# Performance work log

Hardware: AMD Instinct MI355X
Metric: run time of the kernel (lower is better)

## Reference

```python
import jax, jax.numpy as jnp
import numpy as np

N = 262144  # total points
D = 256     # embedding dim
S = 8       # number of subbatches
L = 64      # instance labels per subbatch (label id range)
DELTA_V = 0.5
DELTA_D = 1.5


def setup_inputs() -> dict:
    key = jax.random.key(0)
    k1, k2, k3 = jax.random.split(key, 3)
    outputs = jax.random.normal(k1, (N, D), dtype=jnp.float32)
    labels = jax.random.randint(k2, (N,), 0, L, dtype=jnp.int32)
    subbatch_indices = jax.random.randint(k3, (N,), 0, S, dtype=jnp.int32)
    return {"outputs": outputs, "labels": labels, "subbatch_indices": subbatch_indices}


def reference(outputs, labels, subbatch_indices):
    n = outputs.shape[0]
    # normalize embeddings (L2 norm per point, matching torch.linalg.norm axis=1)
    x = outputs / (jnp.linalg.norm(outputs, axis=1) + 1e-8)[:, None]

    # combined segment id: (subbatch, label) -> subbatch*L + label
    seg = subbatch_indices * L + labels  # [N]
    num_seg = S * L

    ones = jnp.ones((n,), dtype=x.dtype)
    counts = jax.ops.segment_sum(ones, seg, num_segments=num_seg)        # [S*L] Nm per (sb,label)
    sums = jax.ops.segment_sum(x, seg, num_segments=num_seg)             # [S*L, D]
    mus = sums / jnp.maximum(counts, 1.0)[:, None]                        # centroids
    present = counts > 0                                                  # [S*L]
    M = jnp.sum(present.reshape(S, L).astype(x.dtype), axis=1)            # [S] unique labels per subbatch

    # ---- pull term: sum_m sum_{i in m} relu(||mu_m - x_i||_1 - dv)^2 / (M*Nm) ----
    mu_pt = mus[seg]                                                      # [N, D]
    d1 = jnp.sum(jnp.abs(mu_pt - x), axis=1)                              # [N] L1 dist to own centroid
    pull_pt = jax.nn.relu(d1 - DELTA_V) ** 2                              # weights are all 1.0
    denom = M[subbatch_indices] * counts[seg]                             # [N] M_sb * Nm
    L_pull = jax.ops.segment_sum(pull_pt / denom, subbatch_indices, num_segments=S)  # [S]

    # ---- push term: pairwise centroid L1 distances within each subbatch ----
    mus_s = mus.reshape(S, L, D)
    pres = present.reshape(S, L)
    dist = jnp.sum(jnp.abs(mus_s[:, :, None, :] - mus_s[:, None, :, :]), axis=-1)  # [S,L,L]
    pairmask = pres[:, :, None] & pres[:, None, :]
    pairmask = pairmask & (~jnp.eye(L, dtype=bool))[None]
    push = jnp.sum(jnp.where(pairmask, jax.nn.relu(2.0 * DELTA_D - dist) ** 2, 0.0), axis=(1, 2))
    L_push = push / jnp.maximum(M * (M - 1.0), 1.0)                        # [S]

    # only subbatches with M > 1 contribute; divide by B = total number of points
    valid = M > 1.0
    loss = jnp.sum(jnp.where(valid, L_pull + L_push, 0.0)) / n
    return loss
```

## Files before the change

### kernel.cpp

```cpp
#include <hip/hip_runtime.h>
#include <hip/hip_bf16.h>

#define DIM 256
#define NSB 8
#define NLBL 64
#define NSEG (NSB * NLBL)
#define BPS 4

__global__ void k_hist(const int* __restrict__ labels, const int* __restrict__ sbidx,
                       int* __restrict__ seg_out, int* __restrict__ counts, int n) {
    __shared__ int bins[NSEG];
    for (int i = threadIdx.x; i < NSEG; i += blockDim.x) bins[i] = 0;
    __syncthreads();
    int stride = gridDim.x * blockDim.x;
    for (int p = blockIdx.x * blockDim.x + threadIdx.x; p < n; p += stride) {
        int seg = sbidx[p] * NLBL + labels[p];
        seg_out[p] = seg;
        atomicAdd(&bins[seg], 1);
    }
    __syncthreads();
    for (int i = threadIdx.x; i < NSEG; i += blockDim.x)
        if (bins[i] > 0) atomicAdd(&counts[i], bins[i]);
}

__global__ void k_scan(const int* __restrict__ counts, int* __restrict__ offsets,
                       int* __restrict__ cursors, float* __restrict__ Mvals) {
    int lane = threadIdx.x;
    int carry = 0;
    for (int c = 0; c < NSB; c++) {
        int idx = c * 64 + lane;
        int v = counts[idx];
        int incl = v;
        #pragma unroll
        for (int m = 1; m < 64; m <<= 1) {
            int t = __shfl_up(incl, m, 64);
            if (lane >= m) incl += t;
        }
        int excl = carry + incl - v;
        offsets[idx] = excl;
        cursors[idx] = excl;
        carry += __shfl(incl, 63, 64);
        unsigned long long b = __ballot(v > 0);
        if (lane == 0) Mvals[c] = (float)__popcll(b);
    }
}

__global__ void k_scatter(const int* __restrict__ seg, int* __restrict__ cursors,
                          int* __restrict__ sorted, int n) {
    int stride = gridDim.x * blockDim.x;
    for (int p = blockIdx.x * blockDim.x + threadIdx.x; p < n; p += stride) {
        int pos = atomicAdd(&cursors[seg[p]], 1);
        sorted[pos] = p;
    }
}

__global__ void k_accum(const float* __restrict__ outp, const int* __restrict__ sorted,
                        const int* __restrict__ offsets, const int* __restrict__ counts,
                        float* __restrict__ partials) {
    int seg = blockIdx.x >> 2;
    int part = blockIdx.x & 3;
    int base = offsets[seg], cnt = counts[seg];
    int chunk = (cnt + BPS - 1) / BPS;
    int lo = base + part * chunk;
    int hi = min(base + cnt, lo + chunk);
    int wv = threadIdx.x >> 6, lane = threadIdx.x & 63;
    float4 acc = {0.f, 0.f, 0.f, 0.f};
    int i = lo + wv;
    int nextp = (i < hi) ? sorted[i] : 0;
    for (; i < hi; i += 4) {
        int p = nextp;
        int ni = i + 4;
        nextp = (ni < hi) ? sorted[ni] : 0;
        float4 v = *reinterpret_cast<const float4*>(outp + (size_t)p * DIM + lane * 4);
        float ss = v.x * v.x + v.y * v.y + v.z * v.z + v.w * v.w;
        #pragma unroll
        for (int m = 32; m >= 1; m >>= 1) ss += __shfl_xor(ss, m, 64);
        float rn = 1.0f / (sqrtf(ss) + 1e-8f);
        acc.x += v.x * rn; acc.y += v.y * rn; acc.z += v.z * rn; acc.w += v.w * rn;
    }
    __shared__ float pl[4][DIM];
    pl[wv][lane * 4 + 0] = acc.x;
    pl[wv][lane * 4 + 1] = acc.y;
    pl[wv][lane * 4 + 2] = acc.z;
    pl[wv][lane * 4 + 3] = acc.w;
    __syncthreads();
    int t = threadIdx.x;
    partials[(size_t)blockIdx.x * DIM + t] = pl[0][t] + pl[1][t] + pl[2][t] + pl[3][t];
}

__global__ void k_mu(const float* __restrict__ partials, const int* __restrict__ counts,
                     float* __restrict__ mus) {
    int seg = blockIdx.x, t = threadIdx.x;
    float s = 0.f;
    #pragma unroll
    for (int b = 0; b < BPS; b++) s += partials[((size_t)seg * BPS + b) * DIM + t];
    mus[(size_t)seg * DIM + t] = s / fmaxf((float)counts[seg], 1.0f);
}

__global__ void k_push(const float* __restrict__ mus, const int* __restrict__ counts,
                       float* __restrict__ pushv) {
    __shared__ float lds[NLBL][DIM + 1];
    int s = blockIdx.x >> 4;
    int chunk = blockIdx.x & 15;
    for (int i = threadIdx.x; i < NLBL * DIM; i += 256) {
        int r = i >> 8, d = i & 255;
        lds[r][d] = mus[((size_t)s * NLBL + r) * DIM + d];
    }
    __syncthreads();
    int pair = chunk * 256 + threadIdx.x;
    int l1 = pair >> 6, l2 = pair & 63;
    float dist = 0.0f;
    #pragma unroll 8
    for (int d = 0; d < DIM; d++) dist += fabsf(lds[l1][d] - lds[l2][d]);
    float v = fmaxf(3.0f - dist, 0.0f);
    v = v * v;
    bool ok = (l1 != l2) && (counts[s * NLBL + l1] > 0) && (counts[s * NLBL + l2] > 0);
    v = ok ? v : 0.0f;
    #pragma unroll
    for (int m = 32; m >= 1; m >>= 1) v += __shfl_xor(v, m, 64);
    __shared__ float wsum[4];
    if ((threadIdx.x & 63) == 0) wsum[threadIdx.x >> 6] = v;
    __syncthreads();
    if (threadIdx.x == 0) atomicAdd(&pushv[s], wsum[0] + wsum[1] + wsum[2] + wsum[3]);
}

__global__ void k_pull(const float* __restrict__ outp, const int* __restrict__ sorted,
                       const int* __restrict__ offsets, const int* __restrict__ counts,
                       const float* __restrict__ mus, const float* __restrict__ Mvals,
                       float* __restrict__ Lpull) {
    int seg = blockIdx.x >> 2;
    int part = blockIdx.x & 3;
    int sb = seg >> 6;
    int base = offsets[seg], cnt = counts[seg];
    if (cnt == 0) return;
    int chunk = (cnt + BPS - 1) / BPS;
    int lo = base + part * chunk;
    int hi = min(base + cnt, lo + chunk);
    int wv = threadIdx.x >> 6, lane = threadIdx.x & 63;
    float4 mu = *reinterpret_cast<const float4*>(mus + (size_t)seg * DIM + lane * 4);
    float psum = 0.f;
    int i = lo + wv;
    int nextp = (i < hi) ? sorted[i] : 0;
    for (; i < hi; i += 4) {
        int p = nextp;
        int ni = i + 4;
        nextp = (ni < hi) ? sorted[ni] : 0;
        float4 v = *reinterpret_cast<const float4*>(outp + (size_t)p * DIM + lane * 4);
        float ss = v.x * v.x + v.y * v.y + v.z * v.z + v.w * v.w;
        #pragma unroll
        for (int m = 32; m >= 1; m >>= 1) ss += __shfl_xor(ss, m, 64);
        float rn = 1.0f / (sqrtf(ss) + 1e-8f);
        float d1 = fabsf(mu.x - v.x * rn) + fabsf(mu.y - v.y * rn) +
                   fabsf(mu.z - v.z * rn) + fabsf(mu.w - v.w * rn);
        #pragma unroll
        for (int m = 32; m >= 1; m >>= 1) d1 += __shfl_xor(d1, m, 64);
        float t = fmaxf(d1 - 0.5f, 0.0f);
        psum += t * t;
    }
    __shared__ float wsum[4];
    if (lane == 0) wsum[wv] = psum;
    __syncthreads();
    if (threadIdx.x == 0) {
        float tot = wsum[0] + wsum[1] + wsum[2] + wsum[3];
        atomicAdd(&Lpull[sb], tot / (Mvals[sb] * (float)cnt));
    }
}

__global__ void k_final(const float* __restrict__ Lpull, const float* __restrict__ pushv,
                        const float* __restrict__ Mvals, float* __restrict__ outv, int n) {
    if (threadIdx.x == 0 && blockIdx.x == 0) {
        float loss = 0.0f;
        for (int s = 0; s < NSB; s++) {
            float M = Mvals[s];
            if (M > 1.0f)
                loss += Lpull[s] + pushv[s] / fmaxf(M * (M - 1.0f), 1.0f);
        }
        outv[0] = loss / (float)n;
    }
}

extern "C" void kernel_launch(void* const* d_in, const int* in_sizes, int n_in,
                              void* d_out, int out_size, void* d_ws, size_t ws_size,
                              hipStream_t stream) {
    const float* outp = (const float*)d_in[0];
    const int* labels = (const int*)d_in[1];
    const int* sbidx = (const int*)d_in[2];
    float* out = (float*)d_out;
    int n = in_sizes[1];

    float* mus = (float*)d_ws;
    float* partials = mus + (size_t)NSEG * DIM;
    int* seg = (int*)(partials + (size_t)NSEG * BPS * DIM);
    int* sorted = seg + n;
    int* counts = sorted + n;
    float* Lpull = (float*)(counts + NSEG);
    float* pushv = Lpull + NSB;
    int* offsets = (int*)(pushv + NSB);
    int* cursors = offsets + NSEG;
    float* Mvals = (float*)(cursors + NSEG);

    hipMemsetAsync(counts, 0, (NSEG + 2 * NSB) * 4, stream);

    k_hist<<<256, 256, 0, stream>>>(labels, sbidx, seg, counts, n);
    k_scan<<<1, 64, 0, stream>>>(counts, offsets, cursors, Mvals);
    k_scatter<<<512, 256, 0, stream>>>(seg, cursors, sorted, n);
    k_accum<<<NSEG * BPS, 256, 0, stream>>>(outp, sorted, offsets, counts, partials);
    k_mu<<<NSEG, DIM, 0, stream>>>(partials, counts, mus);
    k_push<<<NSB * 16, 256, 0, stream>>>(mus, counts, pushv);
    k_pull<<<NSEG * BPS, 256, 0, stream>>>(outp, sorted, offsets, counts, mus, Mvals, Lpull);
    k_final<<<1, 64, 0, stream>>>(Lpull, pushv, Mvals, out, n);
}
```

Baseline: 226.1 us.

## Fuse scan into histogram, merge mu into push, stream pull over points linearly

The prefix scan moves into the histogram kernel using a last-block-done counter, which removes one launch and the seg array write. The histogram and scatter now read labels and subbatch indices directly with int4 vector loads. Centroid finalisation is folded into the push kernel. The pull kernel now reads the embedding matrix sequentially instead of gathering through the sorted index, and normalises per point with precomputed inverse counts. Accum and pull each process two points per wave iteration for more memory-level parallelism. The costs are extra work in the push blocks and LDS atomics in pull.

```diff
diff --git a/kernel.cpp b/kernel.cpp
--- a/kernel.cpp
+++ b/kernel.cpp
@@ -8,49 +8,69 @@
 #define BPS 4
 
 __global__ void k_hist(const int* __restrict__ labels, const int* __restrict__ sbidx,
-                       int* __restrict__ seg_out, int* __restrict__ counts, int n) {
+                       int* __restrict__ counts, int* __restrict__ done,
+                       int* __restrict__ offsets, int* __restrict__ cursors,
+                       float* __restrict__ Mvals, float* __restrict__ invcnt, int n) {
     __shared__ int bins[NSEG];
+    __shared__ int lastFlag;
     for (int i = threadIdx.x; i < NSEG; i += blockDim.x) bins[i] = 0;
     __syncthreads();
-    int stride = gridDim.x * blockDim.x;
-    for (int p = blockIdx.x * blockDim.x + threadIdx.x; p < n; p += stride) {
-        int seg = sbidx[p] * NLBL + labels[p];
-        seg_out[p] = seg;
-        atomicAdd(&bins[seg], 1);
+    int t4 = blockIdx.x * blockDim.x + threadIdx.x;
+    int stride4 = gridDim.x * blockDim.x;
+    for (int q = t4; q * 4 < n; q += stride4) {
+        int4 lb = reinterpret_cast<const int4*>(labels)[q];
+        int4 sb = reinterpret_cast<const int4*>(sbidx)[q];
+        atomicAdd(&bins[sb.x * NLBL + lb.x], 1);
+        atomicAdd(&bins[sb.y * NLBL + lb.y], 1);
+        atomicAdd(&bins[sb.z * NLBL + lb.z], 1);
+        atomicAdd(&bins[sb.w * NLBL + lb.w], 1);
     }
     __syncthreads();
     for (int i = threadIdx.x; i < NSEG; i += blockDim.x)
         if (bins[i] > 0) atomicAdd(&counts[i], bins[i]);
-}
-
-__global__ void k_scan(const int* __restrict__ counts, int* __restrict__ offsets,
-                       int* __restrict__ cursors, float* __restrict__ Mvals) {
-    int lane = threadIdx.x;
-    int carry = 0;
-    for (int c = 0; c < NSB; c++) {
-        int idx = c * 64 + lane;
-        int v = counts[idx];
-        int incl = v;
-        #pragma unroll
-        for (int m = 1; m < 64; m <<= 1) {
-            int t = __shfl_up(incl, m, 64);
-            if (lane >= m) incl += t;
-        }
-        int excl = carry + incl - v;
-        offsets[idx] = excl;
-        cursors[idx] = excl;
-        carry += __shfl(incl, 63, 64);
-        unsigned long long b = __ballot(v > 0);
-        if (lane == 0) Mvals[c] = (float)__popcll(b);
-    }
-}
-
-__global__ void k_scatter(const int* __restrict__ seg, int* __restrict__ cursors,
-                          int* __restrict__ sorted, int n) {
+    __syncthreads();
+    if (threadIdx.x == 0) {
+        __threadfence();
+        int t = atomicAdd(done, 1);
+        lastFlag = (t == (int)gridDim.x - 1) ? 1 : 0;
+    }
+    __syncthreads();
+    if (!lastFlag) return;
+    if (threadIdx.x < 64) {
+        int lane = threadIdx.x;
+        int carry = 0;
+        for (int c = 0; c < NSB; c++) {
+            int idx = c * 64 + lane;
+            int v = atomicAdd(&counts[idx], 0);
+            int incl = v;
+            #pragma unroll
+            for (int m = 1; m < 64; m <<= 1) {
+                int t2 = __shfl_up(incl, m, 64);
+                if (lane >= m) incl += t2;
+            }
+            int excl = carry + incl - v;
+            offsets[idx] = excl;
+            cursors[idx] = excl;
+            invcnt[idx] = 1.0f / fmaxf((float)v, 1.0f);
+            carry += __shfl(incl, 63, 64);
+            unsigned long long b = __ballot(v > 0);
+            if (lane == 0) Mvals[c] = (float)__popcll(b);
+        }
+    }
+}
+
+__global__ void k_scatter(const int* __restrict__ labels, const int* __restrict__ sbidx,
+                          int* __restrict__ cursors, int* __restrict__ sorted, int n) {
+    int t = blockIdx.x * blockDim.x + threadIdx.x;
     int stride = gridDim.x * blockDim.x;
-    for (int p = blockIdx.x * blockDim.x + threadIdx.x; p < n; p += stride) {
-        int pos = atomicAdd(&cursors[seg[p]], 1);
-        sorted[pos] = p;
+    for (int q = t; q * 4 < n; q += stride) {
+        int4 lb = reinterpret_cast<const int4*>(labels)[q];
+        int4 sb = reinterpret_cast<const int4*>(sbidx)[q];
+        int p = q * 4;
+        sorted[atomicAdd(&cursors[sb.x * NLBL + lb.x], 1)] = p;
+        sorted[atomicAdd(&cursors[sb.y * NLBL + lb.y], 1)] = p + 1;
+        sorted[atomicAdd(&cursors[sb.z * NLBL + lb.z], 1)] = p + 2;
+        sorted[atomicAdd(&cursors[sb.w * NLBL + lb.w], 1)] = p + 3;
     }
 }
 
@@ -65,18 +85,31 @@
     int hi = min(base + cnt, lo + chunk);
     int wv = threadIdx.x >> 6, lane = threadIdx.x & 63;
     float4 acc = {0.f, 0.f, 0.f, 0.f};
-    int i = lo + wv;
-    int nextp = (i < hi) ? sorted[i] : 0;
-    for (; i < hi; i += 4) {
-        int p = nextp;
-        int ni = i + 4;
-        nextp = (ni < hi) ? sorted[ni] : 0;
-        float4 v = *reinterpret_cast<const float4*>(outp + (size_t)p * DIM + lane * 4);
-        float ss = v.x * v.x + v.y * v.y + v.z * v.z + v.w * v.w;
+    int i = lo + wv * 2;
+    int p0 = (i < hi) ? sorted[i] : -1;
+    int p1 = (i + 1 < hi) ? sorted[i + 1] : -1;
+    for (; i < hi; i += 8) {
+        int ni = i + 8;
+        int np0 = (ni < hi) ? sorted[ni] : -1;
+        int np1 = (ni + 1 < hi) ? sorted[ni + 1] : -1;
+        float4 v0 = {0.f, 0.f, 0.f, 0.f}, v1 = {0.f, 0.f, 0.f, 0.f};
+        v0 = *reinterpret_cast<const float4*>(outp + (size_t)p0 * DIM + lane * 4);
+        if (p1 >= 0)
+            v1 = *reinterpret_cast<const float4*>(outp + (size_t)p1 * DIM + lane * 4);
+        float ss0 = v0.x * v0.x + v0.y * v0.y + v0.z * v0.z + v0.w * v0.w;
+        float ss1 = v1.x * v1.x + v1.y * v1.y + v1.z * v1.z + v1.w * v1.w;
         #pragma unroll
-        for (int m = 32; m >= 1; m >>= 1) ss += __shfl_xor(ss, m, 64);
-        float rn = 1.0f / (sqrtf(ss) + 1e-8f);
-        acc.x += v.x * rn; acc.y += v.y * rn; acc.z += v.z * rn; acc.w += v.w * rn;
+        for (int m = 32; m >= 1; m >>= 1) {
+            ss0 += __shfl_xor(ss0, m, 64);
+            ss1 += __shfl_xor(ss1, m, 64);
+        }
+        float rn0 = 1.0f / (sqrtf(ss0) + 1e-8f);
+        float rn1 = 1.0f / (sqrtf(ss1) + 1e-8f);
+        acc.x += v0.x * rn0 + v1.x * rn1;
+        acc.y += v0.y * rn0 + v1.y * rn1;
+        acc.z += v0.z * rn0 + v1.z * rn1;
+        acc.w += v0.w * rn0 + v1.w * rn1;
+        p0 = np0; p1 = np1;
     }
     __shared__ float pl[4][DIM];
     pl[wv][lane * 4 + 0] = acc.x;
@@ -88,23 +121,19 @@
     partials[(size_t)blockIdx.x * DIM + t] = pl[0][t] + pl[1][t] + pl[2][t] + pl[3][t];
 }
 
-__global__ void k_mu(const float* __restrict__ partials, const int* __restrict__ counts,
-                     float* __restrict__ mus) {
-    int seg = blockIdx.x, t = threadIdx.x;
-    float s = 0.f;
-    #pragma unroll
-    for (int b = 0; b < BPS; b++) s += partials[((size_t)seg * BPS + b) * DIM + t];
-    mus[(size_t)seg * DIM + t] = s / fmaxf((float)counts[seg], 1.0f);
-}
-
-__global__ void k_push(const float* __restrict__ mus, const int* __restrict__ counts,
-                       float* __restrict__ pushv) {
+__global__ void k_push(const float* __restrict__ partials, const int* __restrict__ counts,
+                       float* __restrict__ mus, float* __restrict__ pushv) {
     __shared__ float lds[NLBL][DIM + 1];
     int s = blockIdx.x >> 4;
     int chunk = blockIdx.x & 15;
     for (int i = threadIdx.x; i < NLBL * DIM; i += 256) {
         int r = i >> 8, d = i & 255;
-        lds[r][d] = mus[((size_t)s * NLBL + r) * DIM + d];
+        int segid = s * NLBL + r;
+        const float* pp = partials + (size_t)segid * BPS * DIM + d;
+        float sum = pp[0] + pp[DIM] + pp[2 * DIM] + pp[3 * DIM];
+        float mu = sum / fmaxf((float)counts[segid], 1.0f);
+        lds[r][d] = mu;
+        if (chunk == 0) mus[(size_t)segid * DIM + d] = mu;
     }
     __syncthreads();
     int pair = chunk * 256 + threadIdx.x;
@@ -124,46 +153,55 @@
     if (threadIdx.x == 0) atomicAdd(&pushv[s], wsum[0] + wsum[1] + wsum[2] + wsum[3]);
 }
 
-__global__ void k_pull(const float* __restrict__ outp, const int* __restrict__ sorted,
-                       const int* __restrict__ offsets, const int* __restrict__ counts,
-                       const float* __restrict__ mus, const float* __restrict__ Mvals,
-                       float* __restrict__ Lpull) {
-    int seg = blockIdx.x >> 2;
-    int part = blockIdx.x & 3;
-    int sb = seg >> 6;
-    int base = offsets[seg], cnt = counts[seg];
-    if (cnt == 0) return;
-    int chunk = (cnt + BPS - 1) / BPS;
-    int lo = base + part * chunk;
-    int hi = min(base + cnt, lo + chunk);
-    int wv = threadIdx.x >> 6, lane = threadIdx.x & 63;
-    float4 mu = *reinterpret_cast<const float4*>(mus + (size_t)seg * DIM + lane * 4);
-    float psum = 0.f;
-    int i = lo + wv;
-    int nextp = (i < hi) ? sorted[i] : 0;
-    for (; i < hi; i += 4) {
-        int p = nextp;
-        int ni = i + 4;
-        nextp = (ni < hi) ? sorted[ni] : 0;
-        float4 v = *reinterpret_cast<const float4*>(outp + (size_t)p * DIM + lane * 4);
-        float ss = v.x * v.x + v.y * v.y + v.z * v.z + v.w * v.w;
+__global__ void k_pull(const float* __restrict__ outp, const int* __restrict__ labels,
+                       const int* __restrict__ sbidx, const float* __restrict__ mus,
+                       const float* __restrict__ invcnt, float* __restrict__ Lpull, int n) {
+    __shared__ float lp[NSB];
+    if (threadIdx.x < NSB) lp[threadIdx.x] = 0.f;
+    __syncthreads();
+    int gtid = blockIdx.x * blockDim.x + threadIdx.x;
+    int w = gtid >> 6;
+    int lane = threadIdx.x & 63;
+    int nw = (gridDim.x * blockDim.x) >> 6;
+    for (int p0 = w * 2; p0 < n; p0 += nw * 2) {
+        int p1 = p0 + 1;
+        bool has1 = p1 < n;
+        float4 x0 = *reinterpret_cast<const float4*>(outp + (size_t)p0 * DIM + lane * 4);
+        float4 x1 = {0.f, 0.f, 0.f, 0.f};
+        if (has1) x1 = *reinterpret_cast<const float4*>(outp + (size_t)p1 * DIM + lane * 4);
+        int seg0 = sbidx[p0] * NLBL + labels[p0];
+        int seg1 = has1 ? (sbidx[p1] * NLBL + labels[p1]) : 0;
+        float4 mu0 = *reinterpret_cast<const float4*>(mus + (size_t)seg0 * DIM + lane * 4);
+        float4 mu1 = *reinterpret_cast<const float4*>(mus + (size_t)seg1 * DIM + lane * 4);
+        float ss0 = x0.x * x0.x + x0.y * x0.y + x0.z * x0.z + x0.w * x0.w;
+        float ss1 = x1.x * x1.x + x1.y * x1.y + x1.z * x1.z + x1.w * x1.w;
         #pragma unroll
-        for (int m = 32; m >= 1; m >>= 1) ss += __shfl_xor(ss, m, 64);
-        float rn = 1.0f / (sqrtf(ss) + 1e-8f);
-        float d1 = fabsf(mu.x - v.x * rn) + fabsf(mu.y - v.y * rn) +
-                   fabsf(mu.z - v.z * rn) + fabsf(mu.w - v.w * rn);
+        for (int m = 32; m >= 1; m >>= 1) {
+            ss0 += __shfl_xor(ss0, m, 64);
+            ss1 += __shfl_xor(ss1, m, 64);
+        }
+        float rn0 = 1.0f / (sqrtf(ss0) + 1e-8f);
+        float rn1 = 1.0f / (sqrtf(ss1) + 1e-8f);
+        float d10 = fabsf(mu0.x - x0.x * rn0) + fabsf(mu0.y - x0.y * rn0) +
+                    fabsf(mu0.z - x0.z * rn0) + fabsf(mu0.w - x0.w * rn0);
+        float d11 = fabsf(mu1.x - x1.x * rn1) + fabsf(mu1.y - x1.y * rn1) +
+                    fabsf(mu1.z - x1.z * rn1) + fabsf(mu1.w - x1.w * rn1);
         #pragma unroll
-        for (int m = 32; m >= 1; m >>= 1) d1 += __shfl_xor(d1, m, 64);
-        float t = fmaxf(d1 - 0.5f, 0.0f);
-        psum += t * t;
-    }
-    __shared__ float wsum[4];
-    if (lane == 0) wsum[wv] = psum;
-    __syncthreads();
-    if (threadIdx.x == 0) {
-        float tot = wsum[0] + wsum[1] + wsum[2] + wsum[3];
-        atomicAdd(&Lpull[sb], tot / (Mvals[sb] * (float)cnt));
-    }
+        for (int m = 32; m >= 1; m >>= 1) {
+            d10 += __shfl_xor(d10, m, 64);
+            d11 += __shfl_xor(d11, m, 64);
+        }
+        if (lane == 0) {
+            float t0 = fmaxf(d10 - 0.5f, 0.f);
+            atomicAdd(&lp[seg0 >> 6], t0 * t0 * invcnt[seg0]);
+            if (has1) {
+                float t1 = fmaxf(d11 - 0.5f, 0.f);
+                atomicAdd(&lp[seg1 >> 6], t1 * t1 * invcnt[seg1]);
+            }
+        }
+    }
+    __syncthreads();
+    if (threadIdx.x < NSB) atomicAdd(&Lpull[threadIdx.x], lp[threadIdx.x]);
 }
 
 __global__ void k_final(const float* __restrict__ Lpull, const float* __restrict__ pushv,
@@ -173,7 +211,7 @@
         for (int s = 0; s < NSB; s++) {
             float M = Mvals[s];
             if (M > 1.0f)
-                loss += Lpull[s] + pushv[s] / fmaxf(M * (M - 1.0f), 1.0f);
+                loss += Lpull[s] / M + pushv[s] / fmaxf(M * (M - 1.0f), 1.0f);
         }
         outv[0] = loss / (float)n;
     }
@@ -188,25 +226,24 @@
     float* out = (float*)d_out;
     int n = in_sizes[1];
 
-    float* mus = (float*)d_ws;
-    float* partials = mus + (size_t)NSEG * DIM;
-    int* seg = (int*)(partials + (size_t)NSEG * BPS * DIM);
-    int* sorted = seg + n;
+    float* partials = (float*)d_ws;
+    float* mus = partials + (size_t)NSEG * BPS * DIM;
+    int* sorted = (int*)(mus + (size_t)NSEG * DIM);
     int* counts = sorted + n;
-    float* Lpull = (float*)(counts + NSEG);
+    int* done = counts + NSEG;
+    float* Lpull = (float*)(done + 1);
     float* pushv = Lpull + NSB;
     int* offsets = (int*)(pushv + NSB);
     int* cursors = offsets + NSEG;
     float* Mvals = (float*)(cursors + NSEG);
-
-    hipMemsetAsync(counts, 0, (NSEG + 2 * NSB) * 4, stream);
-
-    k_hist<<<256, 256, 0, stream>>>(labels, sbidx, seg, counts, n);
-    k_scan<<<1, 64, 0, stream>>>(counts, offsets, cursors, Mvals);
-    k_scatter<<<512, 256, 0, stream>>>(seg, cursors, sorted, n);
+    float* invcnt = Mvals + NSB;
+
+    hipMemsetAsync(counts, 0, (NSEG + 1 + 2 * NSB) * 4, stream);
+
+    k_hist<<<256, 256, 0, stream>>>(labels, sbidx, counts, done, offsets, cursors, Mvals, invcnt, n);
+    k_scatter<<<256, 256, 0, stream>>>(labels, sbidx, cursors, sorted, n);
     k_accum<<<NSEG * BPS, 256, 0, stream>>>(outp, sorted, offsets, counts, partials);
-    k_mu<<<NSEG, DIM, 0, stream>>>(partials, counts, mus);
-    k_push<<<NSB * 16, 256, 0, stream>>>(mus, counts, pushv);
-    k_pull<<<NSEG * BPS, 256, 0, stream>>>(outp, sorted, offsets, counts, mus, Mvals, Lpull);
+    k_push<<<NSB * 16, 256, 0, stream>>>(partials, counts, mus, pushv);
+    k_pull<<<2048, 256, 0, stream>>>(outp, labels, sbidx, mus, invcnt, Lpull, n);
     k_final<<<1, 64, 0, stream>>>(Lpull, pushv, Mvals, out, n);
 }
```

Measured after the change: 231.3 us. +2.3%, slower.
